# Kernel optimization log

Hardware: AMD Instinct MI355X
Metric: run time of the kernel (lower is better)

The kernel has to match this reference:

```python
import jax, jax.numpy as jnp
import numpy as np

B, C, L = 2, 256, 2048   # batch, emb_dim, seq_len
D, H = 64, 8             # d_model (per-head), n_heads
HD = D * H
EPS = 1e-8


def glob_ln(x, gamma, beta):
    # x: (B, C, L); normalize over all non-batch dims, affine over channel dim 1
    mean = jnp.mean(x, axis=(1, 2), keepdims=True)
    var = jnp.mean((x - mean) ** 2, axis=(1, 2), keepdims=True)
    normed = (x - mean) / jnp.sqrt(var + EPS)
    return gamma[None, :, None] * normed + beta[None, :, None]


def pos_encoding(length, dim):
    pos = jnp.arange(length, dtype=jnp.float32)[:, None]
    div = jnp.exp(jnp.arange(0, dim, 2, dtype=jnp.float32) * (-np.log(10000.0) / dim))
    ang = pos * div  # (L, dim/2)
    return jnp.stack([jnp.sin(ang), jnp.cos(ang)], axis=-1).reshape(length, dim)


def setup_inputs() -> dict:
    key = jax.random.key(0)
    ks = jax.random.split(key, 16)
    s_in = 1.0 / np.sqrt(C)
    s_hd = 1.0 / np.sqrt(HD)
    return {
        "x": jax.random.normal(ks[0], (B, C, L), dtype=jnp.float32),
        "Wq": jax.random.uniform(ks[1], (HD, C), minval=-s_in, maxval=s_in),
        "bq": jax.random.uniform(ks[2], (HD,), minval=-s_in, maxval=s_in),
        "Wk": jax.random.uniform(ks[3], (HD, C), minval=-s_in, maxval=s_in),
        "bk": jax.random.uniform(ks[4], (HD,), minval=-s_in, maxval=s_in),
        "Wv": jax.random.uniform(ks[5], (HD, C), minval=-s_in, maxval=s_in),
        "bv": jax.random.uniform(ks[6], (HD,), minval=-s_in, maxval=s_in),
        "Wo": jax.random.uniform(ks[7], (C, HD), minval=-s_hd, maxval=s_hd),
        "bo": jax.random.uniform(ks[8], (C,), minval=-s_hd, maxval=s_hd),
        "g_mha": jnp.ones((C,)), "b_mha": jnp.zeros((C,)),
        "conv_w": jax.random.uniform(ks[9], (C, C), minval=-s_in, maxval=s_in),
        "conv_b": jax.random.uniform(ks[10], (C,), minval=-s_in, maxval=s_in),
        "g_ffn": jnp.ones((C,)), "b_ffn": jnp.zeros((C,)),
        "alpha": jnp.float32(0.25),
        "g_out": jnp.ones((C,)), "b_out": jnp.zeros((C,)),
    }


def reference(x, Wq, bq, Wk, bk, Wv, bv, Wo, bo, g_mha, b_mha,
              conv_w, conv_b, g_ffn, b_ffn, alpha, g_out, b_out):
    scale = 1.0 / np.sqrt(D)
    t = jnp.transpose(x, (0, 2, 1))            # (B, L, C)
    t = t + pos_encoding(L, C)[None]
    # multi-head attention (self)
    q = (scale * (t @ Wq.T + bq)).reshape(B, L, H, D)
    k = (t @ Wk.T + bk).reshape(B, L, H, D)
    v = (t @ Wv.T + bv).reshape(B, L, H, D)
    scores = jnp.einsum('nlhd,nshd->nhls', q, k)  # (B, H, L, L)
    attn = jax.nn.softmax(scores, axis=-1)
    o = jnp.einsum('nhls,nshd->nlhd', attn, v).reshape(B, L, HD)
    t = t + (o @ Wo.T + bo)                    # residual
    y = glob_ln(jnp.transpose(t, (0, 2, 1)), g_mha, b_mha)  # (B, C, L)
    # FFN: 1x1 conv + GlobLN + PReLU
    f = jnp.einsum('bcl,oc->bol', y, conv_w) + conv_b[None, :, None]
    f = glob_ln(f, g_ffn, b_ffn)
    f = jnp.where(f >= 0, f, alpha * f)
    return glob_ln(f + y, g_out, b_out)
```

## Files before the change

### kernel.cpp

```cpp
#include <hip/hip_runtime.h>
#include <hip/hip_bf16.h>
#include <math.h>

#define BB   2
#define CC   256
#define LL   2048
#define DD   64
#define HH   8
#define HDIM 512
#define BLQ  (BB*LL)
#define EPSV 1e-8f
#define QSCALE (0.125f * 1.44269504088896f)

typedef __attribute__((ext_vector_type(8))) short short8;
typedef __attribute__((ext_vector_type(4))) float f32x4;

__device__ __forceinline__ float wred_sum(float v) {
#pragma unroll
    for (int off = 32; off > 0; off >>= 1) v += __shfl_down(v, off, 64);
    return v;
}
__device__ __forceinline__ unsigned pk(float a, float b) {
    __hip_bfloat162 h = __float22bfloat162_rn(make_float2(a, b));
    union { __hip_bfloat162 h; unsigned u; } c; c.h = h;
    return c.u;
}
__device__ __forceinline__ short8 ld_frag(const unsigned short* p) {
    union { short8 v; uint2 u[2]; } f;
    f.u[0] = *(const uint2*)p;
    f.u[1] = *(const uint2*)(p + 4);
    return f.v;
}

__global__ __launch_bounds__(256) void k_prep(const float* __restrict__ x,
                                              const float* __restrict__ Wq, const float* __restrict__ Wk,
                                              const float* __restrict__ Wv, const float* __restrict__ Wo,
                                              const float* __restrict__ Wc,
                                              float* __restrict__ t,
                                              unsigned short* __restrict__ tb,
                                              unsigned short* __restrict__ dqkv,
                                              unsigned short* __restrict__ dWo,
                                              unsigned short* __restrict__ dWc) {
    int bid = blockIdx.x;
    int tid = threadIdx.x;
    if (bid >= 256) {
        int idx = ((bid - 256) * 256 + tid) * 4;
        const float* s; unsigned short* d;
        if (idx < 131072)      { s = Wq + idx;          d = dqkv + idx; }
        else if (idx < 262144) { s = Wk + idx - 131072; d = dqkv + idx; }
        else if (idx < 393216) { s = Wv + idx - 262144; d = dqkv + idx; }
        else if (idx < 524288) { s = Wo + idx - 393216; d = dWo + idx - 393216; }
        else                   { s = Wc + idx - 524288; d = dWc + idx - 524288; }
        float4 v = *(const float4*)s;
        uint2 u; u.x = pk(v.x, v.y); u.y = pk(v.z, v.w);
        *(uint2*)d = u;
        return;
    }
    __shared__ float tr[64][65];
    int l0 = (bid & 31) * 64, c0 = ((bid >> 5) & 3) * 64, b = bid >> 7;
    int r = tid >> 2, q = tid & 3;
#pragma unroll
    for (int p = 0; p < 4; ++p) {
        int lc = 4 * (q + 4 * p);
        float4 v = *(const float4*)&x[((size_t)(b * CC + c0 + r)) * LL + l0 + lc];
        tr[lc + 0][r] = v.x; tr[lc + 1][r] = v.y; tr[lc + 2][r] = v.z; tr[lc + 3][r] = v.w;
    }
    __syncthreads();
    int lg = l0 + r;
#pragma unroll
    for (int p = 0; p < 4; ++p) {
        int cc = 4 * (q + 4 * p);
        float4 v = *(const float4*)&tr[r][cc];
        float pe[4];
#pragma unroll
        for (int i = 0; i < 4; ++i) {
            int cg = c0 + cc + i;
            float freq = __expf((float)(cg & ~1) * (-9.210340371976184f / (float)CC));
            float ang = (float)lg * freq;
            pe[i] = (cg & 1) ? __cosf(ang) : __sinf(ang);
        }
        v.x += pe[0]; v.y += pe[1]; v.z += pe[2]; v.w += pe[3];
        size_t o = ((size_t)(b * LL + lg)) * CC + c0 + cc;
        *(float4*)&t[o] = v;
        uint2 u; u.x = pk(v.x, v.y); u.y = pk(v.z, v.w);
        *(uint2*)&tb[o] = u;
    }
}

#define MLDK 68
__global__ __launch_bounds__(256) void k_mm(const unsigned short* __restrict__ A,
                                            const unsigned short* __restrict__ W,
                                            const float* __restrict__ b0,
                                            const float* __restrict__ b1,
                                            const float* __restrict__ b2,
                                            const float* resid,
                                            float* out, unsigned short* outb,
                                            float* pstat,
                                            int mode, int M, int N, int K) {
    __shared__ unsigned short As[2][64][MLDK];
    __shared__ unsigned short Ws[2][64][MLDK];
    __shared__ float rs[4][2];
    int tid = threadIdx.x;
    int w = tid >> 6, lane = tid & 63, g = lane >> 4, qi = lane & 15;
    int bm = blockIdx.x * 64, bn = blockIdx.y * 64;
    int wr = w >> 1, wc = w & 1;
    int srow = tid >> 2, sq = tid & 3;
    bool vseg = (mode == 1) && (bn >= 1024);
    f32x4 acc[2][2];
    acc[0][0] = acc[0][1] = acc[1][0] = acc[1][1] = (f32x4){0.f, 0.f, 0.f, 0.f};
    uint4 ra[2], rw[2];
#pragma unroll
    for (int p = 0; p < 2; ++p) {
        ra[p] = *(const uint4*)&A[(size_t)(bm + srow) * K + (sq + 4 * p) * 8];
        rw[p] = *(const uint4*)&W[(size_t)(bn + srow) * K + (sq + 4 * p) * 8];
    }
    int nt = K >> 6;
    for (int it = 0; it < nt; ++it) {
        int buf = it & 1;
#pragma unroll
        for (int p = 0; p < 2; ++p) {
            *(uint2*)&As[buf][srow][(sq + 4 * p) * 8]     = make_uint2(ra[p].x, ra[p].y);
            *(uint2*)&As[buf][srow][(sq + 4 * p) * 8 + 4] = make_uint2(ra[p].z, ra[p].w);
            *(uint2*)&Ws[buf][srow][(sq + 4 * p) * 8]     = make_uint2(rw[p].x, rw[p].y);
            *(uint2*)&Ws[buf][srow][(sq + 4 * p) * 8 + 4] = make_uint2(rw[p].z, rw[p].w);
        }
        __syncthreads();
        if (it + 1 < nt) {
            int k0 = (it + 1) << 6;
#pragma unroll
            for (int p = 0; p < 2; ++p) {
                ra[p] = *(const uint4*)&A[(size_t)(bm + srow) * K + k0 + (sq + 4 * p) * 8];
                rw[p] = *(const uint4*)&W[(size_t)(bn + srow) * K + k0 + (sq + 4 * p) * 8];
            }
        }
#pragma unroll
        for (int c = 0; c < 2; ++c) {
            short8 wf0 = ld_frag(&Ws[buf][wr * 32 + 0  + qi][c * 32 + 8 * g]);
            short8 wf1 = ld_frag(&Ws[buf][wr * 32 + 16 + qi][c * 32 + 8 * g]);
            short8 af0 = ld_frag(&As[buf][wc * 32 + 0  + qi][c * 32 + 8 * g]);
            short8 af1 = ld_frag(&As[buf][wc * 32 + 16 + qi][c * 32 + 8 * g]);
            if (!vseg) {
                acc[0][0] = __builtin_amdgcn_mfma_f32_16x16x32_bf16(wf0, af0, acc[0][0], 0, 0, 0);
                acc[0][1] = __builtin_amdgcn_mfma_f32_16x16x32_bf16(wf0, af1, acc[0][1], 0, 0, 0);
                acc[1][0] = __builtin_amdgcn_mfma_f32_16x16x32_bf16(wf1, af0, acc[1][0], 0, 0, 0);
                acc[1][1] = __builtin_amdgcn_mfma_f32_16x16x32_bf16(wf1, af1, acc[1][1], 0, 0, 0);
            } else {
                acc[0][0] = __builtin_amdgcn_mfma_f32_16x16x32_bf16(af0, wf0, acc[0][0], 0, 0, 0);
                acc[0][1] = __builtin_amdgcn_mfma_f32_16x16x32_bf16(af0, wf1, acc[0][1], 0, 0, 0);
                acc[1][0] = __builtin_amdgcn_mfma_f32_16x16x32_bf16(af1, wf0, acc[1][0], 0, 0, 0);
                acc[1][1] = __builtin_amdgcn_mfma_f32_16x16x32_bf16(af1, wf1, acc[1][1], 0, 0, 0);
            }
        }
    }
    if (mode == 0) {
        float s = 0.f, s2 = 0.f;
#pragma unroll
        for (int fi = 0; fi < 2; ++fi)
#pragma unroll
            for (int fj = 0; fj < 2; ++fj) {
                int n0 = bn + wr * 32 + fi * 16 + 4 * g;
                int m  = bm + wc * 32 + fj * 16 + qi;
                float4 bi = *(const float4*)&b0[n0];
                float4 v;
                v.x = acc[fi][fj][0] + bi.x; v.y = acc[fi][fj][1] + bi.y;
                v.z = acc[fi][fj][2] + bi.z; v.w = acc[fi][fj][3] + bi.w;
                if (resid) {
                    float4 rv = *(const float4*)&resid[(size_t)m * N + n0];
                    v.x += rv.x; v.y += rv.y; v.z += rv.z; v.w += rv.w;
                }
                *(float4*)&out[(size_t)m * N + n0] = v;
                s  += (v.x + v.y) + (v.z + v.w);
                s2 += v.x * v.x + v.y * v.y + v.z * v.z + v.w * v.w;
            }
        if (pstat) {
            s = wred_sum(s); s2 = wred_sum(s2);
            if (lane == 0) { rs[w][0] = s; rs[w][1] = s2; }
            __syncthreads();
            if (tid == 0) {
                int bid = blockIdx.y * gridDim.x + blockIdx.x;
                pstat[bid * 2 + 0] = rs[0][0] + rs[1][0] + rs[2][0] + rs[3][0];
                pstat[bid * 2 + 1] = rs[0][1] + rs[1][1] + rs[2][1] + rs[3][1];
            }
        }
    } else if (!vseg) {
        int seg = bn >> 9;
        const float* bs = seg ? b1 : b0;
        float sc = seg ? 1.f : QSCALE;
#pragma unroll
        for (int fi = 0; fi < 2; ++fi)
#pragma unroll
            for (int fj = 0; fj < 2; ++fj) {
                int nn0 = (bn & 511) + wr * 32 + fi * 16 + 4 * g;
                int m   = bm + wc * 32 + fj * 16 + qi;
                int b = m >> 11, l = m & (LL - 1);
                int h = nn0 >> 6, d0 = nn0 & 63;
                float4 bi = *(const float4*)&bs[nn0];
                uint2 u;
                u.x = pk(sc * (acc[fi][fj][0] + bi.x), sc * (acc[fi][fj][1] + bi.y));
                u.y = pk(sc * (acc[fi][fj][2] + bi.z), sc * (acc[fi][fj][3] + bi.w));
                *(uint2*)&outb[(size_t)seg * 2097152 +
                               (((size_t)(b * HH + h)) * LL + l) * DD + d0] = u;
            }
    } else {
#pragma unroll
        for (int fi = 0; fi < 2; ++fi)
#pragma unroll
            for (int fj = 0; fj < 2; ++fj) {
                int m0 = bm + wc * 32 + fi * 16 + 4 * g;
                int nn = (bn & 511) + wr * 32 + fj * 16 + qi;
                int b = m0 >> 11, l0 = m0 & (LL - 1);
                int h = nn >> 6, d = nn & 63;
                float bi = b2[nn];
                uint2 u;
                u.x = pk(acc[fi][fj][0] + bi, acc[fi][fj][1] + bi);
                u.y = pk(acc[fi][fj][2] + bi, acc[fi][fj][3] + bi);
                *(uint2*)&outb[(size_t)2 * 2097152 +
                               (((size_t)(b * HH + h)) * DD + d) * LL + l0] = u;
            }
    }
}

#define LDK 68
__global__ __launch_bounds__(256) void k_attn(const unsigned short* __restrict__ QKV,
                                              unsigned short* __restrict__ o) {
    int h = blockIdx.y, b = blockIdx.z;
    int tid = threadIdx.x;
    int w = tid >> 6, lane = tid & 63, g = lane >> 4, qi = lane & 15;
    int q0 = blockIdx.x * 64 + w * 16;
    __shared__ unsigned short Ks[2][64][LDK];
    __shared__ unsigned short Vts[2][64][LDK];
    __shared__ unsigned short Pw[4][16][LDK];
    const size_t bh = (size_t)(b * HH + h);
    const unsigned short* Qg = QKV + bh * LL * DD;
    const unsigned short* Kg = QKV + 2097152 + bh * LL * DD;
    const unsigned short* Vg = QKV + (size_t)2 * 2097152 + bh * DD * LL;

    short8 qf[2];
#pragma unroll
    for (int c = 0; c < 2; ++c)
        qf[c] = *(const short8*)&Qg[(size_t)(q0 + qi) * DD + c * 32 + 8 * g];
    short8 ones;
#pragma unroll
    for (int i = 0; i < 8; ++i) ones[i] = (short)0x3F80;

    f32x4 ot[5];
#pragma unroll
    for (int db = 0; db < 5; ++db) ot[db] = (f32x4){0.f, 0.f, 0.f, 0.f};
    float m = -INFINITY;

    int srow = tid >> 2, sq = tid & 3;
    uint4 kr[2], vr[2];
#pragma unroll
    for (int p = 0; p < 2; ++p) {
        kr[p] = *(const uint4*)&Kg[(size_t)srow * DD + (sq + 4 * p) * 8];
        vr[p] = *(const uint4*)&Vg[(size_t)srow * LL + (sq + 4 * p) * 8];
    }
    for (int it = 0; it < LL / 64; ++it) {
        int buf = it & 1;
#pragma unroll
        for (int p = 0; p < 2; ++p) {
            *(uint2*)&Ks[buf][srow][(sq + 4 * p) * 8]      = make_uint2(kr[p].x, kr[p].y);
            *(uint2*)&Ks[buf][srow][(sq + 4 * p) * 8 + 4]  = make_uint2(kr[p].z, kr[p].w);
            *(uint2*)&Vts[buf][srow][(sq + 4 * p) * 8]     = make_uint2(vr[p].x, vr[p].y);
            *(uint2*)&Vts[buf][srow][(sq + 4 * p) * 8 + 4] = make_uint2(vr[p].z, vr[p].w);
        }
        __syncthreads();
        if (it + 1 < LL / 64) {
            int s1 = (it + 1) * 64;
#pragma unroll
            for (int p = 0; p < 2; ++p) {
                kr[p] = *(const uint4*)&Kg[(size_t)(s1 + srow) * DD + (sq + 4 * p) * 8];
                vr[p] = *(const uint4*)&Vg[(size_t)srow * LL + s1 + (sq + 4 * p) * 8];
            }
        }
        f32x4 st[4];
        __builtin_amdgcn_s_setprio(1);
#pragma unroll
        for (int sb = 0; sb < 4; ++sb) {
            f32x4 a = (f32x4){0.f, 0.f, 0.f, 0.f};
#pragma unroll
            for (int c = 0; c < 2; ++c) {
                short8 kf = ld_frag(&Ks[buf][sb * 16 + qi][c * 32 + 8 * g]);
                a = __builtin_amdgcn_mfma_f32_16x16x32_bf16(kf, qf[c], a, 0, 0, 0);
            }
            st[sb] = a;
        }
        __builtin_amdgcn_s_setprio(0);
        float t0 = fmaxf(fmaxf(st[0][0], st[0][1]), fmaxf(st[0][2], st[0][3]));
        float t1 = fmaxf(fmaxf(st[1][0], st[1][1]), fmaxf(st[1][2], st[1][3]));
        float t2 = fmaxf(fmaxf(st[2][0], st[2][1]), fmaxf(st[2][2], st[2][3]));
        float t3 = fmaxf(fmaxf(st[3][0], st[3][1]), fmaxf(st[3][2], st[3][3]));
        float tmax = fmaxf(fmaxf(t0, t1), fmaxf(t2, t3));
        tmax = fmaxf(tmax, __shfl_xor(tmax, 16, 64));
        tmax = fmaxf(tmax, __shfl_xor(tmax, 32, 64));
        if (!__all(tmax - m <= 8.f)) {
            float mnew = fmaxf(m, tmax);
            float corr = exp2f(m - mnew);
            m = mnew;
#pragma unroll
            for (int db = 0; db < 5; ++db)
#pragma unroll
                for (int r = 0; r < 4; ++r) ot[db][r] *= corr;
        }
#pragma unroll
        for (int sb = 0; sb < 4; ++sb) {
            float p0 = exp2f(st[sb][0] - m);
            float p1 = exp2f(st[sb][1] - m);
            float p2 = exp2f(st[sb][2] - m);
            float p3 = exp2f(st[sb][3] - m);
            uint2 w2; w2.x = pk(p0, p1); w2.y = pk(p2, p3);
            *(uint2*)&Pw[w][qi][sb * 16 + 4 * g] = w2;
        }
        __builtin_amdgcn_s_setprio(1);
#pragma unroll
        for (int sc = 0; sc < 2; ++sc) {
            short8 pf = ld_frag(&Pw[w][qi][sc * 32 + 8 * g]);
            ot[4] = __builtin_amdgcn_mfma_f32_16x16x32_bf16(ones, pf, ot[4], 0, 0, 0);
#pragma unroll
            for (int db = 0; db < 4; ++db) {
                short8 vf = ld_frag(&Vts[buf][db * 16 + qi][sc * 32 + 8 * g]);
                ot[db] = __builtin_amdgcn_mfma_f32_16x16x32_bf16(vf, pf, ot[db], 0, 0, 0);
            }
        }
        __builtin_amdgcn_s_setprio(0);
    }
    float rinv = 1.f / ot[4][0];
#pragma unroll
    for (int db = 0; db < 4; ++db) {
        int d0 = db * 16 + 4 * g;
        uint2 u;
        u.x = pk(ot[db][0] * rinv, ot[db][1] * rinv);
        u.y = pk(ot[db][2] * rinv, ot[db][3] * rinv);
        *(uint2*)&o[((size_t)(b * LL + q0 + qi)) * HDIM + h * DD + d0] = u;
    }
}

__global__ __launch_bounds__(256) void k_ln(const float* in,
                                            const float* __restrict__ g,
                                            const float* __restrict__ be,
                                            const float* __restrict__ pin,
                                            const float* __restrict__ add,
                                            const float* __restrict__ alpha_ptr,
                                            float* out, unsigned short* outb,
                                            float* pout) {
    __shared__ float rs[4][2];
    int tid = threadIdx.x;
    int b = blockIdx.x >> 9;
    float s = 0.f, s2 = 0.f;
    if (tid < 128) {
        int pidx = (tid >> 5) * 64 + b * 32 + (tid & 31);
        s  = pin[pidx * 2 + 0];
        s2 = pin[pidx * 2 + 1];
    }
    s = wred_sum(s); s2 = wred_sum(s2);
    if ((tid & 63) == 0 && tid < 128) { rs[tid >> 6][0] = s; rs[tid >> 6][1] = s2; }
    __syncthreads();
    float S = rs[0][0] + rs[1][0], S2 = rs[0][1] + rs[1][1];
    float mean = S / (float)(CC * LL);
    float inv  = rsqrtf(S2 / (float)(CC * LL) - mean * mean + EPSV);

    int idx = (blockIdx.x * 256 + tid) * 4;
    int c = idx & (CC - 1);
    float4 v  = *(const float4*)&in[idx];
    float4 gg = *(const float4*)&g[c];
    float4 bb = *(const float4*)&be[c];
    v.x = (v.x - mean) * inv * gg.x + bb.x;
    v.y = (v.y - mean) * inv * gg.y + bb.y;
    v.z = (v.z - mean) * inv * gg.z + bb.z;
    v.w = (v.w - mean) * inv * gg.w + bb.w;
    if (alpha_ptr) {
        float al = alpha_ptr[0];
        v.x = v.x >= 0.f ? v.x : al * v.x;
        v.y = v.y >= 0.f ? v.y : al * v.y;
        v.z = v.z >= 0.f ? v.z : al * v.z;
        v.w = v.w >= 0.f ? v.w : al * v.w;
    }
    if (add) {
        float4 a = *(const float4*)&add[idx];
        v.x += a.x; v.y += a.y; v.z += a.z; v.w += a.w;
    }
    *(float4*)&out[idx] = v;
    if (outb) {
        uint2 u; u.x = pk(v.x, v.y); u.y = pk(v.z, v.w);
        *(uint2*)&outb[idx] = u;
    }
    if (pout) {
        float os  = (v.x + v.y) + (v.z + v.w);
        float os2 = v.x * v.x + v.y * v.y + v.z * v.z + v.w * v.w;
        os = wred_sum(os); os2 = wred_sum(os2);
        __syncthreads();
        if ((tid & 63) == 0) { rs[tid >> 6][0] = os; rs[tid >> 6][1] = os2; }
        __syncthreads();
        if (tid == 0) {
            pout[blockIdx.x * 2 + 0] = rs[0][0] + rs[1][0] + rs[2][0] + rs[3][0];
            pout[blockIdx.x * 2 + 1] = rs[0][1] + rs[1][1] + rs[2][1] + rs[3][1];
        }
    }
}

__global__ __launch_bounds__(256) void k_ln_t(const float* __restrict__ in,
                                              const float* __restrict__ g,
                                              const float* __restrict__ be,
                                              const float* __restrict__ pin,
                                              float* __restrict__ out) {
    __shared__ float tr[64][65];
    __shared__ float rs[4][2];
    int l0 = blockIdx.x * 64, c0 = blockIdx.y * 64, b = blockIdx.z;
    int tid = threadIdx.x, r = tid >> 2, q = tid & 3;
    float s  = pin[(b * 512 + tid) * 2 + 0] + pin[(b * 512 + 256 + tid) * 2 + 0];
    float s2 = pin[(b * 512 + tid) * 2 + 1] + pin[(b * 512 + 256 + tid) * 2 + 1];
    s = wred_sum(s); s2 = wred_sum(s2);
    if ((tid & 63) == 0) { rs[tid >> 6][0] = s; rs[tid >> 6][1] = s2; }
    __syncthreads();
    float S = rs[0][0] + rs[1][0] + rs[2][0] + rs[3][0];
    float S2 = rs[0][1] + rs[1][1] + rs[2][1] + rs[3][1];
    float mean = S / (float)(CC * LL);
    float inv  = rsqrtf(S2 / (float)(CC * LL) - mean * mean + EPSV);
#pragma unroll
    for (int p = 0; p < 4; ++p) {
        int cc = 4 * (q + 4 * p);
        float4 v  = *(const float4*)&in[((size_t)(b * LL + l0 + r)) * CC + c0 + cc];
        float4 gg = *(const float4*)&g[c0 + cc];
        float4 bb = *(const float4*)&be[c0 + cc];
        tr[cc + 0][r] = (v.x - mean) * inv * gg.x + bb.x;
        tr[cc + 1][r] = (v.y - mean) * inv * gg.y + bb.y;
        tr[cc + 2][r] = (v.z - mean) * inv * gg.z + bb.z;
        tr[cc + 3][r] = (v.w - mean) * inv * gg.w + bb.w;
    }
    __syncthreads();
#pragma unroll
    for (int p = 0; p < 4; ++p) {
        int ll = 4 * (q + 4 * p);
        float4 v = *(const float4*)&tr[r][ll];
        *(float4*)&out[((size_t)(b * CC + c0 + r)) * LL + l0 + ll] = v;
    }
}

extern "C" void kernel_launch(void* const* d_in, const int* in_sizes, int n_in,
                              void* d_out, int out_size, void* d_ws, size_t ws_size,
                              hipStream_t stream) {
    const float* x      = (const float*)d_in[0];
    const float* Wq     = (const float*)d_in[1];
    const float* bq     = (const float*)d_in[2];
    const float* Wk     = (const float*)d_in[3];
    const float* bk     = (const float*)d_in[4];
    const float* Wv     = (const float*)d_in[5];
    const float* bv     = (const float*)d_in[6];
    const float* Wo     = (const float*)d_in[7];
    const float* bo     = (const float*)d_in[8];
    const float* g_mha  = (const float*)d_in[9];
    const float* b_mha  = (const float*)d_in[10];
    const float* conv_w = (const float*)d_in[11];
    const float* conv_b = (const float*)d_in[12];
    const float* g_ffn  = (const float*)d_in[13];
    const float* b_ffn  = (const float*)d_in[14];
    const float* alpha  = (const float*)d_in[15];
    const float* g_out  = (const float*)d_in[16];
    const float* b_out  = (const float*)d_in[17];
    float* out = (float*)d_out;

    float* ws = (float*)d_ws;
    float* t             = ws;
    unsigned short* tb   = (unsigned short*)(ws + 1048576);
    unsigned short* QKVb = (unsigned short*)(ws + 1572864);
    float* f             = ws + 1572864;
    unsigned short* ybf  = (unsigned short*)(ws + 2621440);
    unsigned short* obuf = (unsigned short*)(ws + 4718592);
    unsigned short* Wqkvb= (unsigned short*)(ws + 5767168);
    unsigned short* Wob  = (unsigned short*)(ws + 5963776);
    unsigned short* Wcb  = (unsigned short*)(ws + 6029312);
    float* pstatA        = ws + 6062080;
    float* pstatB        = ws + 6062592;
    float* pstatC        = ws + 6063104;

    k_prep<<<832, 256, 0, stream>>>(x, Wq, Wk, Wv, Wo, conv_w, t, tb, Wqkvb, Wob, Wcb);

    dim3 gqkv(BLQ / 64, 1536 / 64);
    k_mm<<<gqkv, 256, 0, stream>>>(tb, Wqkvb, bq, bk, bv, nullptr, nullptr, QKVb,
                                   nullptr, 1, BLQ, 1536, CC);

    dim3 gattn(LL / 64, HH, BB);
    k_attn<<<gattn, 256, 0, stream>>>(QKVb, obuf);

    dim3 go(BLQ / 64, CC / 64);
    k_mm<<<go, 256, 0, stream>>>(obuf, Wob, bo, nullptr, nullptr, t, t, nullptr,
                                 pstatA, 0, BLQ, CC, HDIM);

    k_ln<<<1024, 256, 0, stream>>>(t, g_mha, b_mha, pstatA, nullptr, nullptr,
                                   t, ybf, nullptr);

    k_mm<<<go, 256, 0, stream>>>(ybf, Wcb, conv_b, nullptr, nullptr, nullptr, f, nullptr,
                                 pstatB, 0, BLQ, CC, CC);

    k_ln<<<1024, 256, 0, stream>>>(f, g_ffn, b_ffn, pstatB, t, alpha,
                                   f, nullptr, pstatC);

    k_ln_t<<<dim3(LL / 64, CC / 64, BB), 256, 0, stream>>>(f, g_out, b_out, pstatC, out);
}
```

Baseline: 96.31 us.

## Rewrite attention as single-wave 32x32 MFMA kernel with register-resident P

The attention kernel now runs one wavefront per block, each handling 32 queries with 32x32x16 bf16 MFMAs. K and V fragments are loaded straight from global memory into registers, so there is no LDS staging and no block barrier. The P matrix is repacked in registers with v_permlane32_swap instead of going through shared memory. The row sum is accumulated in scalar registers rather than with an extra ones-MFMA. The aim is to remove LDS traffic, syncs and the redundant MFMA, but each wave now re-reads K and V from global/L2 with no sharing between waves, which may make the kernel memory-bound.

```diff
diff --git a/kernel.cpp b/kernel.cpp
--- a/kernel.cpp
+++ b/kernel.cpp
@@ -14,6 +14,7 @@
 
 typedef __attribute__((ext_vector_type(8))) short short8;
 typedef __attribute__((ext_vector_type(4))) float f32x4;
+typedef __attribute__((ext_vector_type(16))) float f32x16;
 
 __device__ __forceinline__ float wred_sum(float v) {
 #pragma unroll
@@ -21,9 +22,20 @@
     return v;
 }
 __device__ __forceinline__ unsigned pk(float a, float b) {
-    __hip_bfloat162 h = __float22bfloat162_rn(make_float2(a, b));
-    union { __hip_bfloat162 h; unsigned u; } c; c.h = h;
-    return c.u;
+    unsigned r;
+    asm("v_cvt_pk_bf16_f32 %0, %1, %2" : "=v"(r) : "v"(a), "v"(b));
+    return r;
+}
+__device__ __forceinline__ void pswap(unsigned &x, unsigned &y) {
+    asm("v_permlane32_swap_b32 %0, %1" : "+v"(x), "+v"(y));
+}
+__device__ __forceinline__ short8 mk8(unsigned x0, unsigned x1, unsigned x2, unsigned x3) {
+    union { short8 v; unsigned u[4]; } r;
+    r.u[0] = x0; r.u[1] = x1; r.u[2] = x2; r.u[3] = x3;
+    return r.v;
+}
+__device__ __forceinline__ short8 as8(uint4 x) {
+    union { short8 v; uint4 u; } r; r.u = x; return r.v;
 }
 __device__ __forceinline__ short8 ld_frag(const unsigned short* p) {
     union { short8 v; uint2 u[2]; } f;
@@ -220,118 +232,94 @@
     }
 }
 
-#define LDK 68
-__global__ __launch_bounds__(256) void k_attn(const unsigned short* __restrict__ QKV,
-                                              unsigned short* __restrict__ o) {
+__global__ __launch_bounds__(64) void k_attn(const unsigned short* __restrict__ QKV,
+                                             unsigned short* __restrict__ o) {
     int h = blockIdx.y, b = blockIdx.z;
-    int tid = threadIdx.x;
-    int w = tid >> 6, lane = tid & 63, g = lane >> 4, qi = lane & 15;
-    int q0 = blockIdx.x * 64 + w * 16;
-    __shared__ unsigned short Ks[2][64][LDK];
-    __shared__ unsigned short Vts[2][64][LDK];
-    __shared__ unsigned short Pw[4][16][LDK];
+    int lane = threadIdx.x;
+    int lo31 = lane & 31, hi = lane >> 5;
+    int q0 = blockIdx.x * 32;
     const size_t bh = (size_t)(b * HH + h);
     const unsigned short* Qg = QKV + bh * LL * DD;
     const unsigned short* Kg = QKV + 2097152 + bh * LL * DD;
     const unsigned short* Vg = QKV + (size_t)2 * 2097152 + bh * DD * LL;
 
-    short8 qf[2];
-#pragma unroll
-    for (int c = 0; c < 2; ++c)
-        qf[c] = *(const short8*)&Qg[(size_t)(q0 + qi) * DD + c * 32 + 8 * g];
-    short8 ones;
-#pragma unroll
-    for (int i = 0; i < 8; ++i) ones[i] = (short)0x3F80;
-
-    f32x4 ot[5];
-#pragma unroll
-    for (int db = 0; db < 5; ++db) ot[db] = (f32x4){0.f, 0.f, 0.f, 0.f};
-    float m = -INFINITY;
-
-    int srow = tid >> 2, sq = tid & 3;
-    uint4 kr[2], vr[2];
-#pragma unroll
-    for (int p = 0; p < 2; ++p) {
-        kr[p] = *(const uint4*)&Kg[(size_t)srow * DD + (sq + 4 * p) * 8];
-        vr[p] = *(const uint4*)&Vg[(size_t)srow * LL + (sq + 4 * p) * 8];
-    }
-    for (int it = 0; it < LL / 64; ++it) {
-        int buf = it & 1;
-#pragma unroll
-        for (int p = 0; p < 2; ++p) {
-            *(uint2*)&Ks[buf][srow][(sq + 4 * p) * 8]      = make_uint2(kr[p].x, kr[p].y);
-            *(uint2*)&Ks[buf][srow][(sq + 4 * p) * 8 + 4]  = make_uint2(kr[p].z, kr[p].w);
-            *(uint2*)&Vts[buf][srow][(sq + 4 * p) * 8]     = make_uint2(vr[p].x, vr[p].y);
-            *(uint2*)&Vts[buf][srow][(sq + 4 * p) * 8 + 4] = make_uint2(vr[p].z, vr[p].w);
-        }
-        __syncthreads();
-        if (it + 1 < LL / 64) {
-            int s1 = (it + 1) * 64;
-#pragma unroll
-            for (int p = 0; p < 2; ++p) {
-                kr[p] = *(const uint4*)&Kg[(size_t)(s1 + srow) * DD + (sq + 4 * p) * 8];
-                vr[p] = *(const uint4*)&Vg[(size_t)srow * LL + s1 + (sq + 4 * p) * 8];
-            }
-        }
-        f32x4 st[4];
-        __builtin_amdgcn_s_setprio(1);
-#pragma unroll
-        for (int sb = 0; sb < 4; ++sb) {
-            f32x4 a = (f32x4){0.f, 0.f, 0.f, 0.f};
-#pragma unroll
-            for (int c = 0; c < 2; ++c) {
-                short8 kf = ld_frag(&Ks[buf][sb * 16 + qi][c * 32 + 8 * g]);
-                a = __builtin_amdgcn_mfma_f32_16x16x32_bf16(kf, qf[c], a, 0, 0, 0);
-            }
-            st[sb] = a;
-        }
-        __builtin_amdgcn_s_setprio(0);
-        float t0 = fmaxf(fmaxf(st[0][0], st[0][1]), fmaxf(st[0][2], st[0][3]));
-        float t1 = fmaxf(fmaxf(st[1][0], st[1][1]), fmaxf(st[1][2], st[1][3]));
-        float t2 = fmaxf(fmaxf(st[2][0], st[2][1]), fmaxf(st[2][2], st[2][3]));
-        float t3 = fmaxf(fmaxf(st[3][0], st[3][1]), fmaxf(st[3][2], st[3][3]));
+    short8 qf[4];
+#pragma unroll
+    for (int c = 0; c < 4; ++c)
+        qf[c] = *(const short8*)&Qg[(size_t)(q0 + lo31) * DD + c * 16 + 8 * hi];
+
+    f32x16 o0, o1;
+#pragma unroll
+    for (int r = 0; r < 16; ++r) { o0[r] = 0.f; o1[r] = 0.f; }
+    float den = 0.f, m = -INFINITY;
+
+    uint4 kfr[4];
+#pragma unroll
+    for (int c = 0; c < 4; ++c)
+        kfr[c] = *(const uint4*)&Kg[(size_t)lo31 * DD + c * 16 + 8 * hi];
+
+#pragma unroll 2
+    for (int t = 0; t < LL / 32; ++t) {
+        int s0 = t * 32;
+        uint4 vfr[2][2];
+#pragma unroll
+        for (int dt = 0; dt < 2; ++dt)
+#pragma unroll
+            for (int kf = 0; kf < 2; ++kf)
+                vfr[dt][kf] = *(const uint4*)&Vg[(size_t)(dt * 32 + lo31) * LL + s0 + kf * 16 + 8 * hi];
+        f32x16 st;
+#pragma unroll
+        for (int r = 0; r < 16; ++r) st[r] = 0.f;
+#pragma unroll
+        for (int c = 0; c < 4; ++c)
+            st = __builtin_amdgcn_mfma_f32_32x32x16_bf16(as8(kfr[c]), qf[c], st, 0, 0, 0);
+#pragma unroll
+        for (int c = 0; c < 4; ++c)
+            kfr[c] = *(const uint4*)&Kg[(size_t)(s0 + 32 + lo31) * DD + c * 16 + 8 * hi];
+        float t0 = fmaxf(fmaxf(st[0], st[1]),  fmaxf(st[2], st[3]));
+        float t1 = fmaxf(fmaxf(st[4], st[5]),  fmaxf(st[6], st[7]));
+        float t2 = fmaxf(fmaxf(st[8], st[9]),  fmaxf(st[10], st[11]));
+        float t3 = fmaxf(fmaxf(st[12], st[13]), fmaxf(st[14], st[15]));
         float tmax = fmaxf(fmaxf(t0, t1), fmaxf(t2, t3));
-        tmax = fmaxf(tmax, __shfl_xor(tmax, 16, 64));
         tmax = fmaxf(tmax, __shfl_xor(tmax, 32, 64));
         if (!__all(tmax - m <= 8.f)) {
             float mnew = fmaxf(m, tmax);
             float corr = exp2f(m - mnew);
             m = mnew;
-#pragma unroll
-            for (int db = 0; db < 5; ++db)
-#pragma unroll
-                for (int r = 0; r < 4; ++r) ot[db][r] *= corr;
-        }
-#pragma unroll
-        for (int sb = 0; sb < 4; ++sb) {
-            float p0 = exp2f(st[sb][0] - m);
-            float p1 = exp2f(st[sb][1] - m);
-            float p2 = exp2f(st[sb][2] - m);
-            float p3 = exp2f(st[sb][3] - m);
-            uint2 w2; w2.x = pk(p0, p1); w2.y = pk(p2, p3);
-            *(uint2*)&Pw[w][qi][sb * 16 + 4 * g] = w2;
-        }
-        __builtin_amdgcn_s_setprio(1);
-#pragma unroll
-        for (int sc = 0; sc < 2; ++sc) {
-            short8 pf = ld_frag(&Pw[w][qi][sc * 32 + 8 * g]);
-            ot[4] = __builtin_amdgcn_mfma_f32_16x16x32_bf16(ones, pf, ot[4], 0, 0, 0);
-#pragma unroll
-            for (int db = 0; db < 4; ++db) {
-                short8 vf = ld_frag(&Vts[buf][db * 16 + qi][sc * 32 + 8 * g]);
-                ot[db] = __builtin_amdgcn_mfma_f32_16x16x32_bf16(vf, pf, ot[db], 0, 0, 0);
-            }
-        }
-        __builtin_amdgcn_s_setprio(0);
-    }
-    float rinv = 1.f / ot[4][0];
-#pragma unroll
-    for (int db = 0; db < 4; ++db) {
-        int d0 = db * 16 + 4 * g;
+            den *= corr;
+#pragma unroll
+            for (int r = 0; r < 16; ++r) { o0[r] *= corr; o1[r] *= corr; }
+        }
+        float p[16];
+#pragma unroll
+        for (int r = 0; r < 16; ++r) { p[r] = exp2f(st[r] - m); den += p[r]; }
+        unsigned pa = pk(p[0], p[1]),  pb = pk(p[2], p[3]);
+        unsigned pc = pk(p[4], p[5]),  pd = pk(p[6], p[7]);
+        pswap(pc, pa); pswap(pd, pb);
+        unsigned pe = pk(p[8], p[9]),  pf = pk(p[10], p[11]);
+        unsigned pg = pk(p[12], p[13]), ph = pk(p[14], p[15]);
+        pswap(pg, pe); pswap(ph, pf);
+        short8 pb0 = mk8(pa, pb, pc, pd);
+        short8 pb1 = mk8(pe, pf, pg, ph);
+        o0 = __builtin_amdgcn_mfma_f32_32x32x16_bf16(as8(vfr[0][0]), pb0, o0, 0, 0, 0);
+        o0 = __builtin_amdgcn_mfma_f32_32x32x16_bf16(as8(vfr[0][1]), pb1, o0, 0, 0, 0);
+        o1 = __builtin_amdgcn_mfma_f32_32x32x16_bf16(as8(vfr[1][0]), pb0, o1, 0, 0, 0);
+        o1 = __builtin_amdgcn_mfma_f32_32x32x16_bf16(as8(vfr[1][1]), pb1, o1, 0, 0, 0);
+    }
+    den += __shfl_xor(den, 32, 64);
+    float rinv = 1.f / den;
+    size_t base = ((size_t)(b * LL + q0 + lo31)) * HDIM + h * DD;
+#pragma unroll
+    for (int j = 0; j < 4; ++j) {
+        int d0 = 8 * j + 4 * hi;
         uint2 u;
-        u.x = pk(ot[db][0] * rinv, ot[db][1] * rinv);
-        u.y = pk(ot[db][2] * rinv, ot[db][3] * rinv);
-        *(uint2*)&o[((size_t)(b * LL + q0 + qi)) * HDIM + h * DD + d0] = u;
+        u.x = pk(o0[4 * j + 0] * rinv, o0[4 * j + 1] * rinv);
+        u.y = pk(o0[4 * j + 2] * rinv, o0[4 * j + 3] * rinv);
+        *(uint2*)&o[base + d0] = u;
+        uint2 u1;
+        u1.x = pk(o1[4 * j + 0] * rinv, o1[4 * j + 1] * rinv);
+        u1.y = pk(o1[4 * j + 2] * rinv, o1[4 * j + 3] * rinv);
+        *(uint2*)&o[base + 32 + d0] = u1;
     }
 }
 
@@ -479,8 +467,8 @@
     k_mm<<<gqkv, 256, 0, stream>>>(tb, Wqkvb, bq, bk, bv, nullptr, nullptr, QKVb,
                                    nullptr, 1, BLQ, 1536, CC);
 
-    dim3 gattn(LL / 64, HH, BB);
-    k_attn<<<gattn, 256, 0, stream>>>(QKVb, obuf);
+    dim3 gattn(LL / 32, HH, BB);
+    k_attn<<<gattn, 64, 0, stream>>>(QKVb, obuf);
 
     dim3 go(BLQ / 64, CC / 64);
     k_mm<<<go, 256, 0, stream>>>(obuf, Wob, bo, nullptr, nullptr, t, t, nullptr,
```

Result: slower. 121.7 us (+26.4%).

## Compute softmax row sum with VALU instead of ones-MFMA, reorder attention grid

Applied to the files above, without the earlier changes.

Drops the extra MFMA that multiplied P by a ones vector to get the softmax denominator. The sum is now accumulated in registers from the fp32 probabilities and reduced across lanes with shuffles at the end. The attention grid is reordered so consecutive blocks cover different heads and batches, which changes the order K/V tiles are read through L2. The bf16 pack now uses inline v_cvt_pk_bf16_f32 assembly. The trade-off is extra VALU adds in place of one MFMA per chunk, and the denominator is summed from unrounded fp32 rather than bf16 values.

```diff
diff --git a/kernel.cpp b/kernel.cpp
--- a/kernel.cpp
+++ b/kernel.cpp
@@ -21,9 +21,9 @@
     return v;
 }
 __device__ __forceinline__ unsigned pk(float a, float b) {
-    __hip_bfloat162 h = __float22bfloat162_rn(make_float2(a, b));
-    union { __hip_bfloat162 h; unsigned u; } c; c.h = h;
-    return c.u;
+    unsigned r;
+    asm("v_cvt_pk_bf16_f32 %0, %1, %2" : "=v"(r) : "v"(a), "v"(b));
+    return r;
 }
 __device__ __forceinline__ short8 ld_frag(const unsigned short* p) {
     union { short8 v; uint2 u[2]; } f;
@@ -223,30 +223,27 @@
 #define LDK 68
 __global__ __launch_bounds__(256) void k_attn(const unsigned short* __restrict__ QKV,
                                               unsigned short* __restrict__ o) {
-    int h = blockIdx.y, b = blockIdx.z;
+    int bh = blockIdx.x;
+    int h = bh & 7, b = bh >> 3;
     int tid = threadIdx.x;
     int w = tid >> 6, lane = tid & 63, g = lane >> 4, qi = lane & 15;
-    int q0 = blockIdx.x * 64 + w * 16;
+    int q0 = blockIdx.y * 64 + w * 16;
     __shared__ unsigned short Ks[2][64][LDK];
     __shared__ unsigned short Vts[2][64][LDK];
     __shared__ unsigned short Pw[4][16][LDK];
-    const size_t bh = (size_t)(b * HH + h);
-    const unsigned short* Qg = QKV + bh * LL * DD;
-    const unsigned short* Kg = QKV + 2097152 + bh * LL * DD;
-    const unsigned short* Vg = QKV + (size_t)2 * 2097152 + bh * DD * LL;
+    const unsigned short* Qg = QKV + (size_t)bh * LL * DD;
+    const unsigned short* Kg = QKV + 2097152 + (size_t)bh * LL * DD;
+    const unsigned short* Vg = QKV + (size_t)2 * 2097152 + (size_t)bh * DD * LL;
 
     short8 qf[2];
 #pragma unroll
     for (int c = 0; c < 2; ++c)
         qf[c] = *(const short8*)&Qg[(size_t)(q0 + qi) * DD + c * 32 + 8 * g];
-    short8 ones;
-#pragma unroll
-    for (int i = 0; i < 8; ++i) ones[i] = (short)0x3F80;
-
-    f32x4 ot[5];
-#pragma unroll
-    for (int db = 0; db < 5; ++db) ot[db] = (f32x4){0.f, 0.f, 0.f, 0.f};
-    float m = -INFINITY;
+
+    f32x4 ot[4];
+#pragma unroll
+    for (int db = 0; db < 4; ++db) ot[db] = (f32x4){0.f, 0.f, 0.f, 0.f};
+    float m = -INFINITY, sum = 0.f;
 
     int srow = tid >> 2, sq = tid & 3;
     uint4 kr[2], vr[2];
@@ -297,34 +294,38 @@
             float mnew = fmaxf(m, tmax);
             float corr = exp2f(m - mnew);
             m = mnew;
-#pragma unroll
-            for (int db = 0; db < 5; ++db)
+            sum *= corr;
+#pragma unroll
+            for (int db = 0; db < 4; ++db)
 #pragma unroll
                 for (int r = 0; r < 4; ++r) ot[db][r] *= corr;
         }
+        float ps = 0.f;
 #pragma unroll
         for (int sb = 0; sb < 4; ++sb) {
             float p0 = exp2f(st[sb][0] - m);
             float p1 = exp2f(st[sb][1] - m);
             float p2 = exp2f(st[sb][2] - m);
             float p3 = exp2f(st[sb][3] - m);
+            ps += (p0 + p1) + (p2 + p3);
             uint2 w2; w2.x = pk(p0, p1); w2.y = pk(p2, p3);
             *(uint2*)&Pw[w][qi][sb * 16 + 4 * g] = w2;
         }
+        sum += ps;
         __builtin_amdgcn_s_setprio(1);
 #pragma unroll
-        for (int sc = 0; sc < 2; ++sc) {
-            short8 pf = ld_frag(&Pw[w][qi][sc * 32 + 8 * g]);
-            ot[4] = __builtin_amdgcn_mfma_f32_16x16x32_bf16(ones, pf, ot[4], 0, 0, 0);
-#pragma unroll
-            for (int db = 0; db < 4; ++db) {
+        for (int db = 0; db < 4; ++db)
+#pragma unroll
+            for (int sc = 0; sc < 2; ++sc) {
                 short8 vf = ld_frag(&Vts[buf][db * 16 + qi][sc * 32 + 8 * g]);
+                short8 pf = ld_frag(&Pw[w][qi][sc * 32 + 8 * g]);
                 ot[db] = __builtin_amdgcn_mfma_f32_16x16x32_bf16(vf, pf, ot[db], 0, 0, 0);
             }
-        }
         __builtin_amdgcn_s_setprio(0);
     }
-    float rinv = 1.f / ot[4][0];
+    sum += __shfl_xor(sum, 16, 64);
+    sum += __shfl_xor(sum, 32, 64);
+    float rinv = 1.f / sum;
 #pragma unroll
     for (int db = 0; db < 4; ++db) {
         int d0 = db * 16 + 4 * g;
@@ -479,7 +480,7 @@
     k_mm<<<gqkv, 256, 0, stream>>>(tb, Wqkvb, bq, bk, bv, nullptr, nullptr, QKVb,
                                    nullptr, 1, BLQ, 1536, CC);
 
-    dim3 gattn(LL / 64, HH, BB);
+    dim3 gattn(HH * BB, LL / 64);
     k_attn<<<gattn, 256, 0, stream>>>(QKVb, obuf);
 
     dim3 go(BLQ / 64, CC / 64);
```

After: 97.61 us. About the same (+1.3%).
